# Optimization experiments

Measured on AMD Instinct MI355X. Metric: run time of the kernel, lower is better.

## Reference

```python
import jax, jax.numpy as jnp
import numpy as np

PUNISHMENT = 0.01
SMOOTHNESS_PUNISHMENT = 0.05
N, H, W, C = 32, 512, 512, 3


def setup_inputs() -> dict:
    key = jax.random.key(0)
    k1, k2, k3, k4 = jax.random.split(key, 4)
    # atanh needs |x|<1
    image = (jax.random.uniform(k1, (1, H, W, C), jnp.float32) * 1.8 - 0.9)
    mask = (jax.random.uniform(k2, (1, H, W, C)) > 0.5).astype(jnp.float32)
    inter = jax.random.normal(k3, (1, H, W, C), jnp.float32) * 0.1
    # projective transforms near identity: [a0,a1,a2,b0,b1,b2,c0,c1] (tfa convention)
    ident = jnp.array([1, 0, 0, 0, 1, 0, 0, 0], jnp.float32)
    scale = jnp.array([0.05, 0.05, 5.0, 0.05, 0.05, 5.0, 0.0, 0.0], jnp.float32)
    transforms = ident + jax.random.normal(k4, (N, 8), jnp.float32) * scale
    return {"image": image, "mask": mask, "inter": inter, "transforms": transforms}


def _bilinear_transform(img, transforms):
    """tfa.image.transform (BILINEAR, constant fill 0) of one image under N transforms.
    img: [H,W,C]; transforms: [N,8]. Returns [N,H,W,C].
    Fuses the batch duplication: samples the single shared image per transform."""
    H_, W_, _ = img.shape
    y, x = jnp.meshgrid(jnp.arange(H_, dtype=img.dtype), jnp.arange(W_, dtype=img.dtype), indexing='ij')
    a0, a1, a2, b0, b1, b2, c0, c1 = [transforms[:, i][:, None, None] for i in range(8)]
    denom = c0 * x + c1 * y + 1.0
    sx = (a0 * x + a1 * y + a2) / denom  # [N,H,W] source x
    sy = (b0 * x + b1 * y + b2) / denom  # [N,H,W] source y
    x0 = jnp.floor(sx)
    y0 = jnp.floor(sy)

    def tap(xc, yc):
        valid = (xc >= 0) & (xc <= W_ - 1) & (yc >= 0) & (yc <= H_ - 1)
        xi = jnp.clip(xc, 0, W_ - 1).astype(jnp.int32)
        yi = jnp.clip(yc, 0, H_ - 1).astype(jnp.int32)
        v = img[yi, xi]  # gather -> [N,H,W,C]
        return v * valid[..., None].astype(img.dtype)

    wx = (sx - x0)[..., None]
    wy = (sy - y0)[..., None]
    v00 = tap(x0, y0)
    v01 = tap(x0 + 1, y0)
    v10 = tap(x0, y0 + 1)
    v11 = tap(x0 + 1, y0 + 1)
    top = v00 * (1 - wx) + v01 * wx
    bot = v10 * (1 - wx) + v11 * wx
    return top * (1 - wy) + bot * wy


def reference(image, mask, inter, transforms):
    w_image = jnp.arctanh(image)              # [1,H,W,C]
    masked_inter = mask * inter               # [1,H,W,C]
    # concat-duplicate-to-N + tfa.image.transform, fused into per-transform sampling
    warped = _bilinear_transform(masked_inter[0], transforms)  # [N,H,W,C]
    constrained = jnp.tanh(w_image + warped)  # [N,H,W,C]
    perturbation = image - constrained        # broadcast over N
    distance_l2 = jnp.sqrt(jnp.sum(perturbation * perturbation))
    # faithful slicing over batch/height axes; empty (0) when batch==1, as in TF
    diff = masked_inter[0:-1, 0:-1] - masked_inter[1:, 1:]
    non_smoothness = jnp.sqrt(jnp.sum(diff * diff))
    partial_loss = jnp.array([PUNISHMENT], jnp.float32) * distance_l2 \
        + jnp.array([SMOOTHNESS_PUNISHMENT], jnp.float32) * non_smoothness
    return constrained, partial_loss
```

## Files before the change

### kernel.cpp

```cpp
#include <hip/hip_runtime.h>
#include <math.h>

#define HH 512
#define WW 512
#define NNB 32
constexpr int PIXB = 256;
constexpr int PIX = HH * WW;
constexpr int IMG_ELEMS = PIX * 3;
constexpr int NPB = PIX / PIXB;
constexpr int NBLOCKS = NNB * NPB;

__global__ __launch_bounds__(256) void eot_prep(
    const float* __restrict__ img, const float* __restrict__ mask,
    const float* __restrict__ inter, float* __restrict__ wimg,
    float* __restrict__ masked) {
  int i = blockIdx.x * 256 + threadIdx.x;
  if (i < IMG_ELEMS) {
    float xv = img[i];
    wimg[i] = 0.5f * logf((1.0f + xv) / (1.0f - xv));
    masked[i] = mask[i] * inter[i];
  }
}

__global__ __launch_bounds__(256) void eot_main(
    const float* __restrict__ img, const float* __restrict__ wimg,
    const float* __restrict__ msk, const float* __restrict__ trans,
    float* __restrict__ out, float* __restrict__ partials) {
  const int n = blockIdx.x;
  const int p = blockIdx.y * PIXB + threadIdx.x;

  const float* t = trans + n * 8;
  const float a0 = t[0], a1 = t[1], a2 = t[2];
  const float b0 = t[3], b1 = t[4], b2 = t[5];
  const float c0 = t[6], c1 = t[7];

  const int yy = p >> 9;
  const int xx = p & (WW - 1);
  const float fx = (float)xx, fy = (float)yy;

  const float den = c0 * fx + c1 * fy + 1.0f;
  const float rden = __fdividef(1.0f, den);
  const float sx = (a0 * fx + a1 * fy + a2) * rden;
  const float sy = (b0 * fx + b1 * fy + b2) * rden;

  const float x0f = floorf(sx), y0f = floorf(sy);
  const float wx = sx - x0f, wy = sy - y0f;
  const float x1f = x0f + 1.0f, y1f = y0f + 1.0f;

  const bool vx0 = (x0f >= 0.0f) & (x0f <= (float)(WW - 1));
  const bool vx1 = (x1f >= 0.0f) & (x1f <= (float)(WW - 1));
  const bool vy0 = (y0f >= 0.0f) & (y0f <= (float)(HH - 1));
  const bool vy1 = (y1f >= 0.0f) & (y1f <= (float)(HH - 1));

  const int xi0 = min(max((int)x0f, 0), WW - 1);
  const int xi1 = min(max((int)x1f, 0), WW - 1);
  const int yi0 = min(max((int)y0f, 0), HH - 1);
  const int yi1 = min(max((int)y1f, 0), HH - 1);

  const float f00 = (vx0 & vy0) ? 1.0f : 0.0f;
  const float f01 = (vx1 & vy0) ? 1.0f : 0.0f;
  const float f10 = (vx0 & vy1) ? 1.0f : 0.0f;
  const float f11 = (vx1 & vy1) ? 1.0f : 0.0f;

  const int o00 = (yi0 * WW + xi0) * 3;
  const int o01 = (yi0 * WW + xi1) * 3;
  const int o10 = (yi1 * WW + xi0) * 3;
  const int o11 = (yi1 * WW + xi1) * 3;

  const float omwx = 1.0f - wx, omwy = 1.0f - wy;

  const int pb = p * 3;
  const size_t ob = ((size_t)n * PIX + p) * 3;
  float accv = 0.0f;

#pragma unroll
  for (int c = 0; c < 3; ++c) {
    const float v00 = msk[o00 + c] * f00;
    const float v01 = msk[o01 + c] * f01;
    const float v10 = msk[o10 + c] * f10;
    const float v11 = msk[o11 + c] * f11;
    const float top = v00 * omwx + v01 * wx;
    const float bot = v10 * omwx + v11 * wx;
    const float warped = top * omwy + bot * wy;

    const float a = wimg[pb + c] + warped;
    const float E = __expf(2.0f * a);
    const float con = 1.0f - __fdividef(2.0f, E + 1.0f);

    __builtin_nontemporal_store(con, &out[ob + c]);

    const float pert = img[pb + c] - con;
    accv = fmaf(pert, pert, accv);
  }

#pragma unroll
  for (int off = 32; off > 0; off >>= 1) accv += __shfl_down(accv, off, 64);
  __shared__ float red[4];
  const int lane = threadIdx.x & 63, wid = threadIdx.x >> 6;
  if (lane == 0) red[wid] = accv;
  __syncthreads();
  if (threadIdx.x == 0) {
    partials[blockIdx.y * NNB + blockIdx.x] = red[0] + red[1] + red[2] + red[3];
  }
}

__global__ __launch_bounds__(1024) void eot_finalize(
    const float* __restrict__ partials, float* __restrict__ loss) {
  double s = 0.0;
  for (int i = threadIdx.x; i < NBLOCKS; i += 1024) s += (double)partials[i];
#pragma unroll
  for (int off = 32; off > 0; off >>= 1) s += __shfl_down(s, off, 64);
  __shared__ double red[16];
  const int lane = threadIdx.x & 63, wid = threadIdx.x >> 6;
  if (lane == 0) red[wid] = s;
  __syncthreads();
  if (threadIdx.x == 0) {
    double tot = 0.0;
#pragma unroll
    for (int w = 0; w < 16; ++w) tot += red[w];
    loss[0] = 0.01f * (float)sqrt(tot);
  }
}

extern "C" void kernel_launch(void* const* d_in, const int* in_sizes, int n_in,
                              void* d_out, int out_size, void* d_ws, size_t ws_size,
                              hipStream_t stream) {
  const float* image = (const float*)d_in[0];
  const float* mask  = (const float*)d_in[1];
  const float* inter = (const float*)d_in[2];
  const float* trans = (const float*)d_in[3];
  float* out = (float*)d_out;

  float* partials = (float*)d_ws;
  float* wimg = partials + NBLOCKS;
  float* masked = wimg + IMG_ELEMS;

  eot_prep<<<IMG_ELEMS / 256, 256, 0, stream>>>(image, mask, inter, wimg, masked);

  dim3 grid(NNB, NPB);
  eot_main<<<grid, PIXB, 0, stream>>>(image, wimg, masked, trans, out, partials);

  eot_finalize<<<1, 1024, 0, stream>>>(partials, out + (size_t)NNB * IMG_ELEMS);
}
```

Measured before the change: 154.4 us.

## Loop over transforms per thread, pad masked image to float4, fuse atanh

Each thread now handles one pixel for a group of eight transforms, loading the image and computing atanh once and reusing them across those transforms. The prep kernel writes the masked perturbation as padded float4, so each bilinear tap is a single vector load instead of three scalar loads. Transforms are staged in shared memory, and the grid changes so the slow axis splits the transforms into four groups. This cuts redundant image reads and gather instructions, at the cost of fewer blocks, more work per thread, and writes that are strided by a whole image per loop iteration.

```diff
diff --git a/kernel.cpp b/kernel.cpp
--- a/kernel.cpp
+++ b/kernel.cpp
@@ -7,90 +7,104 @@
 constexpr int PIXB = 256;
 constexpr int PIX = HH * WW;
 constexpr int IMG_ELEMS = PIX * 3;
-constexpr int NPB = PIX / PIXB;
-constexpr int NBLOCKS = NNB * NPB;
+constexpr int NSPLIT = 4;
+constexpr int NPT = NNB / NSPLIT;
+constexpr int PBLK = PIX / PIXB;
+constexpr int NPART = PBLK * NSPLIT;
 
 __global__ __launch_bounds__(256) void eot_prep(
-    const float* __restrict__ img, const float* __restrict__ mask,
-    const float* __restrict__ inter, float* __restrict__ wimg,
-    float* __restrict__ masked) {
-  int i = blockIdx.x * 256 + threadIdx.x;
-  if (i < IMG_ELEMS) {
-    float xv = img[i];
-    wimg[i] = 0.5f * logf((1.0f + xv) / (1.0f - xv));
-    masked[i] = mask[i] * inter[i];
-  }
+    const float* __restrict__ mask, const float* __restrict__ inter,
+    float4* __restrict__ masked4) {
+  const int p = blockIdx.x * 256 + threadIdx.x;
+  const int b = p * 3;
+  masked4[p] = make_float4(mask[b] * inter[b],
+                           mask[b + 1] * inter[b + 1],
+                           mask[b + 2] * inter[b + 2], 0.0f);
 }
 
 __global__ __launch_bounds__(256) void eot_main(
-    const float* __restrict__ img, const float* __restrict__ wimg,
-    const float* __restrict__ msk, const float* __restrict__ trans,
-    float* __restrict__ out, float* __restrict__ partials) {
-  const int n = blockIdx.x;
-  const int p = blockIdx.y * PIXB + threadIdx.x;
+    const float* __restrict__ img, const float4* __restrict__ msk4,
+    const float* __restrict__ trans, float* __restrict__ out,
+    float* __restrict__ partials) {
+  __shared__ float tr[NNB * 8];
+  if (threadIdx.x < NNB * 8) tr[threadIdx.x] = trans[threadIdx.x];
+  __syncthreads();
 
-  const float* t = trans + n * 8;
-  const float a0 = t[0], a1 = t[1], a2 = t[2];
-  const float b0 = t[3], b1 = t[4], b2 = t[5];
-  const float c0 = t[6], c1 = t[7];
-
+  const int p = blockIdx.x * PIXB + threadIdx.x;
   const int yy = p >> 9;
   const int xx = p & (WW - 1);
   const float fx = (float)xx, fy = (float)yy;
+  const int pb = p * 3;
 
-  const float den = c0 * fx + c1 * fy + 1.0f;
-  const float rden = __fdividef(1.0f, den);
-  const float sx = (a0 * fx + a1 * fy + a2) * rden;
-  const float sy = (b0 * fx + b1 * fy + b2) * rden;
+  const float i0 = img[pb], i1 = img[pb + 1], i2 = img[pb + 2];
+  const float w0 = 0.5f * logf((1.0f + i0) / (1.0f - i0));
+  const float w1 = 0.5f * logf((1.0f + i1) / (1.0f - i1));
+  const float w2 = 0.5f * logf((1.0f + i2) / (1.0f - i2));
 
-  const float x0f = floorf(sx), y0f = floorf(sy);
-  const float wx = sx - x0f, wy = sy - y0f;
-  const float x1f = x0f + 1.0f, y1f = y0f + 1.0f;
-
-  const bool vx0 = (x0f >= 0.0f) & (x0f <= (float)(WW - 1));
-  const bool vx1 = (x1f >= 0.0f) & (x1f <= (float)(WW - 1));
-  const bool vy0 = (y0f >= 0.0f) & (y0f <= (float)(HH - 1));
-  const bool vy1 = (y1f >= 0.0f) & (y1f <= (float)(HH - 1));
-
-  const int xi0 = min(max((int)x0f, 0), WW - 1);
-  const int xi1 = min(max((int)x1f, 0), WW - 1);
-  const int yi0 = min(max((int)y0f, 0), HH - 1);
-  const int yi1 = min(max((int)y1f, 0), HH - 1);
-
-  const float f00 = (vx0 & vy0) ? 1.0f : 0.0f;
-  const float f01 = (vx1 & vy0) ? 1.0f : 0.0f;
-  const float f10 = (vx0 & vy1) ? 1.0f : 0.0f;
-  const float f11 = (vx1 & vy1) ? 1.0f : 0.0f;
-
-  const int o00 = (yi0 * WW + xi0) * 3;
-  const int o01 = (yi0 * WW + xi1) * 3;
-  const int o10 = (yi1 * WW + xi0) * 3;
-  const int o11 = (yi1 * WW + xi1) * 3;
-
-  const float omwx = 1.0f - wx, omwy = 1.0f - wy;
-
-  const int pb = p * 3;
-  const size_t ob = ((size_t)n * PIX + p) * 3;
+  const int n0 = blockIdx.y * NPT;
   float accv = 0.0f;
 
-#pragma unroll
-  for (int c = 0; c < 3; ++c) {
-    const float v00 = msk[o00 + c] * f00;
-    const float v01 = msk[o01 + c] * f01;
-    const float v10 = msk[o10 + c] * f10;
-    const float v11 = msk[o11 + c] * f11;
-    const float top = v00 * omwx + v01 * wx;
-    const float bot = v10 * omwx + v11 * wx;
-    const float warped = top * omwy + bot * wy;
+#pragma unroll 2
+  for (int k = 0; k < NPT; ++k) {
+    const int n = n0 + k;
+    const float* t = &tr[n * 8];
+    const float a0 = t[0], a1 = t[1], a2 = t[2];
+    const float b0 = t[3], b1 = t[4], b2 = t[5];
+    const float c0 = t[6], c1 = t[7];
 
-    const float a = wimg[pb + c] + warped;
-    const float E = __expf(2.0f * a);
-    const float con = 1.0f - __fdividef(2.0f, E + 1.0f);
+    const float den = c0 * fx + c1 * fy + 1.0f;
+    const float rden = __fdividef(1.0f, den);
+    const float sx = (a0 * fx + a1 * fy + a2) * rden;
+    const float sy = (b0 * fx + b1 * fy + b2) * rden;
 
-    __builtin_nontemporal_store(con, &out[ob + c]);
+    const float x0f = floorf(sx), y0f = floorf(sy);
+    const float wx = sx - x0f, wy = sy - y0f;
+    const float x1f = x0f + 1.0f, y1f = y0f + 1.0f;
 
-    const float pert = img[pb + c] - con;
-    accv = fmaf(pert, pert, accv);
+    const bool vx0 = (x0f >= 0.0f) & (x0f <= (float)(WW - 1));
+    const bool vx1 = (x1f >= 0.0f) & (x1f <= (float)(WW - 1));
+    const bool vy0 = (y0f >= 0.0f) & (y0f <= (float)(HH - 1));
+    const bool vy1 = (y1f >= 0.0f) & (y1f <= (float)(HH - 1));
+
+    const int xi0 = min(max((int)x0f, 0), WW - 1);
+    const int xi1 = min(max((int)x1f, 0), WW - 1);
+    const int yi0 = min(max((int)y0f, 0), HH - 1);
+    const int yi1 = min(max((int)y1f, 0), HH - 1);
+
+    const float f00 = (vx0 & vy0) ? 1.0f : 0.0f;
+    const float f01 = (vx1 & vy0) ? 1.0f : 0.0f;
+    const float f10 = (vx0 & vy1) ? 1.0f : 0.0f;
+    const float f11 = (vx1 & vy1) ? 1.0f : 0.0f;
+
+    const float4 v00 = msk4[yi0 * WW + xi0];
+    const float4 v01 = msk4[yi0 * WW + xi1];
+    const float4 v10 = msk4[yi1 * WW + xi0];
+    const float4 v11 = msk4[yi1 * WW + xi1];
+
+    const float omwx = 1.0f - wx, omwy = 1.0f - wy;
+    const float c00 = f00 * omwx * omwy;
+    const float c01 = f01 * wx * omwy;
+    const float c10 = f10 * omwx * wy;
+    const float c11 = f11 * wx * wy;
+
+    const float wp0 = v00.x * c00 + v01.x * c01 + v10.x * c10 + v11.x * c11;
+    const float wp1 = v00.y * c00 + v01.y * c01 + v10.y * c10 + v11.y * c11;
+    const float wp2 = v00.z * c00 + v01.z * c01 + v10.z * c10 + v11.z * c11;
+
+    const float E0 = __expf(2.0f * (w0 + wp0));
+    const float E1 = __expf(2.0f * (w1 + wp1));
+    const float E2 = __expf(2.0f * (w2 + wp2));
+    const float con0 = 1.0f - __fdividef(2.0f, E0 + 1.0f);
+    const float con1 = 1.0f - __fdividef(2.0f, E1 + 1.0f);
+    const float con2 = 1.0f - __fdividef(2.0f, E2 + 1.0f);
+
+    float* o = out + (size_t)n * IMG_ELEMS + pb;
+    __builtin_nontemporal_store(con0, o);
+    __builtin_nontemporal_store(con1, o + 1);
+    __builtin_nontemporal_store(con2, o + 2);
+
+    const float p0 = i0 - con0, p1 = i1 - con1, p2 = i2 - con2;
+    accv = fmaf(p0, p0, fmaf(p1, p1, fmaf(p2, p2, accv)));
   }
 
 #pragma unroll
@@ -100,14 +114,14 @@
   if (lane == 0) red[wid] = accv;
   __syncthreads();
   if (threadIdx.x == 0) {
-    partials[blockIdx.y * NNB + blockIdx.x] = red[0] + red[1] + red[2] + red[3];
+    partials[blockIdx.y * PBLK + blockIdx.x] = red[0] + red[1] + red[2] + red[3];
   }
 }
 
 __global__ __launch_bounds__(1024) void eot_finalize(
     const float* __restrict__ partials, float* __restrict__ loss) {
   double s = 0.0;
-  for (int i = threadIdx.x; i < NBLOCKS; i += 1024) s += (double)partials[i];
+  for (int i = threadIdx.x; i < NPART; i += 1024) s += (double)partials[i];
 #pragma unroll
   for (int off = 32; off > 0; off >>= 1) s += __shfl_down(s, off, 64);
   __shared__ double red[16];
@@ -131,14 +145,13 @@
   const float* trans = (const float*)d_in[3];
   float* out = (float*)d_out;
 
-  float* partials = (float*)d_ws;
-  float* wimg = partials + NBLOCKS;
-  float* masked = wimg + IMG_ELEMS;
+  float4* masked4 = (float4*)d_ws;
+  float* partials = (float*)(masked4 + PIX);
 
-  eot_prep<<<IMG_ELEMS / 256, 256, 0, stream>>>(image, mask, inter, wimg, masked);
+  eot_prep<<<PBLK, 256, 0, stream>>>(mask, inter, masked4);
 
-  dim3 grid(NNB, NPB);
-  eot_main<<<grid, PIXB, 0, stream>>>(image, wimg, masked, trans, out, partials);
+  dim3 grid(PBLK, NSPLIT);
+  eot_main<<<grid, PIXB, 0, stream>>>(image, masked4, trans, out, partials);
 
   eot_finalize<<<1, 1024, 0, stream>>>(partials, out + (size_t)NNB * IMG_ELEMS);
 }
```

Result: faster. 145.2 us (-5.9%).
